# Kernel tuning notes

Hardware: AMD Instinct MI355X
Metric: run time of the kernel (lower is better)

The kernel has to match this reference:

```python
import jax, jax.numpy as jnp
import numpy as np

NF = 64   # num_feat
DG = 8    # deformable_groups (also conv groups)
B, H, W = 4, 96, 96
K = 9     # 3x3 kernel positions


def _conv(x, w, b, padding=1, dilation=1, groups=1):
    out = jax.lax.conv_general_dilated(
        x, w, (1, 1), [(padding, padding), (padding, padding)],
        rhs_dilation=(dilation, dilation),
        dimension_numbers=('NCHW', 'OIHW', 'NCHW'),
        feature_group_count=groups)
    return out + b[None, :, None, None]


def _lrelu(t):
    return jnp.where(t >= 0, t, 0.1 * t)


def _cat_align(a, b):
    # channel-interleaved concat: [a0,b0,a1,b1,...]
    Bn, k, h, w = a.shape
    return jnp.stack([a, b], axis=2).reshape(Bn, 2 * k, h, w)


def _deform_conv(x, offset, mask, weight, bias, dilation, padding):
    # DCNv2 modulated deformable conv, stride 1.
    Bn, C, h, w = x.shape
    Cpg = C // DG
    off = offset.reshape(Bn, DG, K, 2, h, w)          # (dy, dx) per group/kernel pos
    m = mask.reshape(Bn, DG, K, h, w)
    ky = (jnp.repeat(jnp.arange(3), 3) * dilation - padding).astype(x.dtype)  # (K,)
    kx = (jnp.tile(jnp.arange(3), 3) * dilation - padding).astype(x.dtype)
    hs = jnp.arange(h, dtype=x.dtype)
    ws = jnp.arange(w, dtype=x.dtype)
    py = off[:, :, :, 0] + ky[None, None, :, None, None] + hs[None, None, None, :, None]
    px = off[:, :, :, 1] + kx[None, None, :, None, None] + ws[None, None, None, None, :]
    y0f = jnp.floor(py); x0f = jnp.floor(px)
    ly = (py - y0f)[:, :, None]  # broadcast over Cpg
    lx = (px - x0f)[:, :, None]
    y0 = y0f.astype(jnp.int32); x0 = x0f.astype(jnp.int32)
    xg = x.reshape(Bn, DG, Cpg, h * w)

    def gather(yi, xi):
        inb = ((yi >= 0) & (yi < h) & (xi >= 0) & (xi < w))
        idx = (jnp.clip(yi, 0, h - 1) * w + jnp.clip(xi, 0, w - 1)).reshape(Bn, DG, 1, K * h * w)
        v = jnp.take_along_axis(xg, jnp.broadcast_to(idx, (Bn, DG, Cpg, K * h * w)), axis=3)
        return v.reshape(Bn, DG, Cpg, K, h, w) * inb[:, :, None].astype(x.dtype)

    v00 = gather(y0, x0); v01 = gather(y0, x0 + 1)
    v10 = gather(y0 + 1, x0); v11 = gather(y0 + 1, x0 + 1)
    val = (v00 * (1 - ly) * (1 - lx) + v01 * (1 - ly) * lx
           + v10 * ly * (1 - lx) + v11 * ly * lx) * m[:, :, None]
    sampled = val.reshape(Bn, C, K, h, w)
    out = jnp.einsum('bckhw,ock->bohw', sampled, weight.reshape(weight.shape[0], C, K))
    return out + bias[None, :, None, None]


def _dcn(x, off_feat, om_w, om_b, w, b, dilation):
    pad = dilation  # int(3/2)*dilation
    out = _conv(off_feat, om_w, om_b, padding=pad, dilation=dilation)
    o1, o2, msk = jnp.split(out, 3, axis=1)
    offset = jnp.concatenate([o1, o2], axis=1)
    mask = jax.nn.sigmoid(msk)
    return _deform_conv(x, offset, mask, w, b, dilation, pad)


def setup_inputs() -> dict:
    key = jax.random.key(0)
    ks = iter(jax.random.split(key, 64))
    def rn(shape, s=0.05):
        return jax.random.normal(next(ks), shape, jnp.float32) * s
    d = {}
    d['nbr_feat'] = jax.random.normal(next(ks), (B, NF, H, W), jnp.float32)
    d['ref_feat'] = jax.random.normal(next(ks), (B, NF, H, W), jnp.float32)
    for lv, has3 in [('l3', False), ('l2', True), ('l1', True)]:
        d[f'oc1_w_{lv}'] = rn((NF, 2 * NF // DG, 3, 3)); d[f'oc1_b_{lv}'] = rn((NF,))
        oc2_in = 2 * NF if has3 else NF
        d[f'oc2_w_{lv}'] = rn((NF, oc2_in // DG, 3, 3)); d[f'oc2_b_{lv}'] = rn((NF,))
        if has3:
            d[f'oc3_w_{lv}'] = rn((NF, NF // DG, 3, 3)); d[f'oc3_b_{lv}'] = rn((NF,))
            d[f'fc_w_{lv}'] = rn((NF, 2 * NF // DG, 3, 3)); d[f'fc_b_{lv}'] = rn((NF,))
        d[f'om_w_{lv}'] = rn((DG * 3 * K, NF, 3, 3), 0.01); d[f'om_b_{lv}'] = rn((DG * 3 * K,), 0.01)
        d[f'dcn_w_{lv}'] = rn((NF, NF, 3, 3)); d[f'dcn_b_{lv}'] = rn((NF,))
    d['cas_oc1_w'] = rn((NF, 2 * NF // DG, 3, 3)); d['cas_oc1_b'] = rn((NF,))
    d['cas_oc2_w'] = rn((NF, NF // DG, 3, 3)); d['cas_oc2_b'] = rn((NF,))
    d['cas_om_w'] = rn((DG * 3 * K, NF, 3, 3), 0.01); d['cas_om_b'] = rn((DG * 3 * K,), 0.01)
    d['cas_w'] = rn((NF, NF, 3, 3)); d['cas_b'] = rn((NF,))
    return d


def reference(nbr_feat, ref_feat,
              oc1_w_l3, oc1_b_l3, oc2_w_l3, oc2_b_l3, om_w_l3, om_b_l3, dcn_w_l3, dcn_b_l3,
              oc1_w_l2, oc1_b_l2, oc2_w_l2, oc2_b_l2, oc3_w_l2, oc3_b_l2, fc_w_l2, fc_b_l2,
              om_w_l2, om_b_l2, dcn_w_l2, dcn_b_l2,
              oc1_w_l1, oc1_b_l1, oc2_w_l1, oc2_b_l1, oc3_w_l1, oc3_b_l1, fc_w_l1, fc_b_l1,
              om_w_l1, om_b_l1, dcn_w_l1, dcn_b_l1,
              cas_oc1_w, cas_oc1_b, cas_oc2_w, cas_oc2_b, cas_om_w, cas_om_b, cas_w, cas_b):
    # level 3 (dilation 5)
    off = _lrelu(_conv(_cat_align(nbr_feat, ref_feat), oc1_w_l3, oc1_b_l3, groups=DG))
    off = _lrelu(_conv(off, oc2_w_l3, oc2_b_l3, groups=DG))
    feat = _lrelu(_dcn(nbr_feat, off, om_w_l3, om_b_l3, dcn_w_l3, dcn_b_l3, 5))
    to, tf = off, feat
    # level 2 (dilation 3)
    off = _lrelu(_conv(_cat_align(nbr_feat, ref_feat), oc1_w_l2, oc1_b_l2, groups=DG))
    off = _lrelu(_conv(_cat_align(off, to), oc2_w_l2, oc2_b_l2, groups=DG))
    off = _lrelu(_conv(off, oc3_w_l2, oc3_b_l2, groups=DG))
    feat = _dcn(nbr_feat, off, om_w_l2, om_b_l2, dcn_w_l2, dcn_b_l2, 3)
    feat = _lrelu(_conv(_cat_align(feat, tf), fc_w_l2, fc_b_l2, groups=DG))
    to, tf = off, feat
    # level 1 (dilation 1), no lrelu on feat
    off = _lrelu(_conv(_cat_align(nbr_feat, ref_feat), oc1_w_l1, oc1_b_l1, groups=DG))
    off = _lrelu(_conv(_cat_align(off, to), oc2_w_l1, oc2_b_l1, groups=DG))
    off = _lrelu(_conv(off, oc3_w_l1, oc3_b_l1, groups=DG))
    feat = _dcn(nbr_feat, off, om_w_l1, om_b_l1, dcn_w_l1, dcn_b_l1, 1)
    feat = _conv(_cat_align(feat, tf), fc_w_l1, fc_b_l1, groups=DG)
    # cascade
    off = _cat_align(feat, ref_feat)
    off = _lrelu(_conv(_lrelu(_conv(off, cas_oc1_w, cas_oc1_b, groups=DG)), cas_oc2_w, cas_oc2_b, groups=DG))
    feat = _lrelu(_dcn(feat, off, cas_om_w, cas_om_b, cas_w, cas_b, 1))
    return feat
```

## Files before the change

kernel.cpp:

```cpp
#include <hip/hip_runtime.h>

#define BATCH 4
#define NFEAT 64
#define DGRP 8
#define HH 96
#define WW 96
#define HWP (HH*WW)

typedef short short4a __attribute__((ext_vector_type(4)));
typedef short short8 __attribute__((ext_vector_type(8)));
typedef float f32x4 __attribute__((ext_vector_type(4)));
typedef float f32x16 __attribute__((ext_vector_type(16)));

__device__ inline short f2bf(float f) {
  union { float f; unsigned u; } v; v.f = f;
  unsigned r = v.u + 0x7fff + ((v.u >> 16) & 1);
  return (short)(r >> 16);
}
__device__ inline float bf2f(short s) {
  return __uint_as_float(((unsigned)(unsigned short)s) << 16);
}

__global__ __launch_bounds__(256) void prep_om(
    const float* __restrict__ s0, const float* __restrict__ s1,
    const float* __restrict__ s2, const float* __restrict__ s3,
    short* __restrict__ dst) {
  int gid = blockIdx.x * 256 + threadIdx.x;
  if (gid >= 4 * 147456) return;
  int t = gid / 147456, r = gid % 147456;
  int tile = r / 18432, r2 = r % 18432;
  int kk = r2 / 512, r3 = r2 % 512;
  int lane = r3 / 8, j = r3 % 8;
  int col = lane & 31, half = lane >> 5;
  int oc = tile * 32 + col;
  int k = kk * 16 + half * 8 + j;
  int p = k >> 6, c = k & 63;
  const float* s = (t == 0) ? s0 : (t == 1) ? s1 : (t == 2) ? s2 : s3;
  float v = (oc < 216) ? s[(size_t)oc * 576 + c * 9 + p] : 0.f;
  dst[gid] = f2bf(v);
}

__global__ __launch_bounds__(256) void prep_dcnw(
    const float* __restrict__ s0, const float* __restrict__ s1,
    const float* __restrict__ s2, const float* __restrict__ s3,
    short* __restrict__ dst) {
  int gid = blockIdx.x * 256 + threadIdx.x;
  if (gid >= 4 * 36864) return;
  int t = gid / 36864, r = gid % 36864;
  int tile = r / 18432, r2 = r % 18432;
  int kk = r2 / 512, r3 = r2 % 512;
  int lane = r3 / 8, j = r3 % 8;
  int col = lane & 31, half = lane >> 5;
  int oc = tile * 32 + col;
  int k = kk * 16 + half * 8 + j;
  int p = k >> 6, c = k & 63;
  const float* s = (t == 0) ? s0 : (t == 1) ? s1 : (t == 2) ? s2 : s3;
  dst[gid] = f2bf(s[(size_t)oc * 576 + c * 9 + p]);
}

struct GwArgs {
  const float* src[12];
  int cat[12];
  int base[13];
};

__global__ __launch_bounds__(256) void prep_gw(GwArgs a, short* __restrict__ dst) {
  int gid = blockIdx.x * 256 + threadIdx.x;
  if (gid >= a.base[12]) return;
  int t = 0;
  while (gid >= a.base[t + 1]) ++t;
  int r = gid - a.base[t];
  const float* s = a.src[t];
  const int tsz = a.cat[t] ? 4608 : 2560;
  int tile = r / tsz, r2 = r % tsz;
  int kk = r2 / 512, r3 = r2 % 512;
  int lane = r3 >> 3, j = r3 & 7;
  int m = lane & 15, quad = lane >> 4;
  int oc = tile * 16 + m;
  int j32 = quad * 8 + j;
  float val = 0.f;
  if (a.cat[t]) {
    int gsel = j32 >> 4, ssel = (j32 >> 3) & 1, ch8 = j32 & 7;
    if (gsel == (m >> 3)) val = s[oc * 144 + (2 * ch8 + ssel) * 9 + kk];
  } else {
    int tapsel = j32 >> 4, gsel = (j32 >> 3) & 1, ch8 = j32 & 7;
    int p = 2 * kk + tapsel;
    if (p < 9 && gsel == (m >> 3)) val = s[oc * 72 + ch8 * 9 + p];
  }
  dst[gid] = f2bf(val);
}

__global__ __launch_bounds__(256) void transpose_bf16(
    const float* __restrict__ in0, short* __restrict__ out0,
    const float* __restrict__ in1, short* __restrict__ out1) {
  const float* in = blockIdx.z ? in1 : in0;
  short* out = blockIdx.z ? out1 : out0;
  __shared__ float s[64][65];
  const int p0 = blockIdx.x * 64;
  const int b = blockIdx.y;
  const int tx = threadIdx.x, ty = threadIdx.y;
  for (int c = ty; c < 64; c += 4)
    s[c][tx] = in[((size_t)b * NFEAT + c) * HWP + p0 + tx];
  __syncthreads();
  for (int p = ty; p < 64; p += 4)
    out[((size_t)b * HWP + p0 + p) * NFEAT + tx] = f2bf(s[tx][p]);
}

template <bool CAT, bool LRELU>
__global__ __launch_bounds__(256) void gconv_mfma(
    const short* __restrict__ in0, const short* __restrict__ in1,
    const short* __restrict__ Wsh, const float* __restrict__ bias,
    short* __restrict__ out) {
  const int lane = threadIdx.x, t = threadIdx.y;
  const int n = lane & 15, quad = lane >> 4;
  const int pixbase = blockIdx.x * 32;
  const int b = blockIdx.y;
  constexpr int NKK = CAT ? 9 : 5;

  short8 A[NKK];
#pragma unroll
  for (int kk = 0; kk < NKK; ++kk)
    A[kk] = *(const short8*)(Wsh + ((size_t)(t * NKK + kk) * 64 + lane) * 8);

  const short* sb;
  if (CAT) {
    sb = ((quad & 1) ? in1 : in0) + (size_t)b * HWP * 64 + (2 * t + (quad >> 1)) * 8;
  } else {
    sb = in0 + (size_t)b * HWP * 64 + (2 * t + (quad & 1)) * 8;
  }

  f32x4 acc[2] = {};
#pragma unroll
  for (int nt = 0; nt < 2; ++nt) {
    const int pix = pixbase + nt * 16 + n;
    const int yp = pix / WW, xp = pix % WW;
#pragma unroll
    for (int kk = 0; kk < NKK; ++kk) {
      const int p = CAT ? kk : (2 * kk + (quad >> 1));
      short8 B = {0, 0, 0, 0, 0, 0, 0, 0};
      if (p < 9) {
        const int sy = yp + p / 3 - 1, sx = xp + p % 3 - 1;
        if (((unsigned)sy < (unsigned)HH) && ((unsigned)sx < (unsigned)WW))
          B = *(const short8*)(sb + (size_t)(sy * WW + sx) * 64);
      }
      acc[nt] = __builtin_amdgcn_mfma_f32_16x16x32_bf16(A[kk], B, acc[nt], 0, 0, 0);
    }
  }

  const int ocb = t * 16 + quad * 4;
  const float b0 = bias[ocb], b1 = bias[ocb + 1], b2 = bias[ocb + 2], b3 = bias[ocb + 3];
#pragma unroll
  for (int nt = 0; nt < 2; ++nt) {
    float v0 = acc[nt][0] + b0, v1 = acc[nt][1] + b1;
    float v2 = acc[nt][2] + b2, v3 = acc[nt][3] + b3;
    if (LRELU) {
      v0 = (v0 >= 0.f) ? v0 : 0.1f * v0;
      v1 = (v1 >= 0.f) ? v1 : 0.1f * v1;
      v2 = (v2 >= 0.f) ? v2 : 0.1f * v2;
      v3 = (v3 >= 0.f) ? v3 : 0.1f * v3;
    }
    short4a pk = {f2bf(v0), f2bf(v1), f2bf(v2), f2bf(v3)};
    *(short4a*)(out + ((size_t)b * HWP + pixbase + nt * 16 + n) * 64 + ocb) = pk;
  }
}

#define BPITCH 324
template <int D>
__global__ __launch_bounds__(256) void omconv_mfma(
    const short* __restrict__ pixT,
    const short* __restrict__ Wsh,
    const float* __restrict__ bias,
    short* __restrict__ out) {
  const int lane = threadIdx.x;
  const int w = threadIdx.y;
  const int lid = w * 64 + lane;
  const int col = lane & 31, half = lane >> 5;
  const int pixbase = blockIdx.x * 64;
  const int b = blockIdx.y;

  __shared__ short Bs[64 * BPITCH];

  const short* aP0 = Wsh + ((size_t)(w * 36) * 64) * 8 + (size_t)lane * 8;
  const short* aP1 = Wsh + ((size_t)((w + 4) * 36) * 64) * 8 + (size_t)lane * 8;
  const short* pixb = pixT + (size_t)b * HWP * 64;

  f32x16 acc00 = {}, acc01 = {}, acc10 = {}, acc11 = {};

  for (int ph = 0; ph < 2; ++ph) {
    const int ntap = ph ? 4 : 5, pbase = ph ? 5 : 0, kbase = ph ? 20 : 0;
    if (ph) __syncthreads();
    const int nchunk = 64 * ntap * 8;
    for (int i = lid; i < nchunk; i += 256) {
      int row = i / (ntap * 8), q = i % (ntap * 8);
      int p = pbase + (q >> 3), c8 = q & 7;
      int pix = pixbase + row;
      int yp = pix / WW, xp = pix % WW;
      int sy = yp + (p / 3 - 1) * D, sx = xp + (p % 3 - 1) * D;
      short4a lo = {0, 0, 0, 0}, hi = {0, 0, 0, 0};
      if (((unsigned)sy < (unsigned)HH) && ((unsigned)sx < (unsigned)WW)) {
        const short* src = pixb + (size_t)(sy * WW + sx) * 64 + c8 * 8;
        lo = *(const short4a*)src;
        hi = *(const short4a*)(src + 4);
      }
      short* dst = Bs + row * BPITCH + q * 8;
      *(short4a*)dst = lo;
      *(short4a*)(dst + 4) = hi;
    }
    __syncthreads();

    const int nkk = ntap * 4;
#pragma unroll 4
    for (int kk = 0; kk < nkk; ++kk) {
      const int kkg = kbase + kk;
      short8 A0 = *(const short8*)(aP0 + (size_t)kkg * 512);
      short8 A1 = *(const short8*)(aP1 + (size_t)kkg * 512);
      const short* b0 = Bs + col * BPITCH + kk * 16 + half * 8;
      const short* b1 = Bs + (32 + col) * BPITCH + kk * 16 + half * 8;
      short4a l0 = *(const short4a*)b0, h0 = *(const short4a*)(b0 + 4);
      short4a l1 = *(const short4a*)b1, h1 = *(const short4a*)(b1 + 4);
      short8 B0 = {l0[0], l0[1], l0[2], l0[3], h0[0], h0[1], h0[2], h0[3]};
      short8 B1 = {l1[0], l1[1], l1[2], l1[3], h1[0], h1[1], h1[2], h1[3]};
      acc00 = __builtin_amdgcn_mfma_f32_32x32x16_bf16(A0, B0, acc00, 0, 0, 0);
      acc01 = __builtin_amdgcn_mfma_f32_32x32x16_bf16(A0, B1, acc01, 0, 0, 0);
      acc10 = __builtin_amdgcn_mfma_f32_32x32x16_bf16(A1, B0, acc10, 0, 0, 0);
      acc11 = __builtin_amdgcn_mfma_f32_32x32x16_bf16(A1, B1, acc11, 0, 0, 0);
    }
  }

  const int pix0 = pixbase + col, pix1 = pixbase + 32 + col;
#pragma unroll
  for (int r = 0; r < 16; ++r) {
    const int rrow = (r & 3) + 8 * (r >> 2) + 4 * half;
    const int oc0 = w * 32 + rrow;
    const int oc1 = (w + 4) * 32 + rrow;
    const float bs0 = bias[oc0];
    out[((size_t)b * 216 + oc0) * HWP + pix0] = f2bf(acc00[r] + bs0);
    out[((size_t)b * 216 + oc0) * HWP + pix1] = f2bf(acc01[r] + bs0);
    if (oc1 < 216) {
      const float bs1 = bias[oc1];
      out[((size_t)b * 216 + oc1) * HWP + pix0] = f2bf(acc10[r] + bs1);
      out[((size_t)b * 216 + oc1) * HWP + pix1] = f2bf(acc11[r] + bs1);
    }
  }
}

template <int D, bool LRELU, bool PMOUT>
__global__ __launch_bounds__(256) void dcn_fused(
    const short* __restrict__ xT,
    const short* __restrict__ om,
    const short* __restrict__ Wd,
    const float* __restrict__ bias,
    void* __restrict__ outv) {
  __shared__ short Ls[36 * 512];
  __shared__ float red[2][64][17];
  const int tx = threadIdx.x, ty = threadIdx.y;
  const int pb = blockIdx.x, b = blockIdx.y;

  {
    const int px = tx, dg = ty;
    const int pix = pb * 32 + px;
    const int yp = pix / WW, xp = pix % WW;
    const size_t bOM = (size_t)b * 216 * HWP;
    const short* xb = xT + (size_t)b * HWP * 64 + dg * 8;
    short* Sp = Ls + (size_t)((dg & 1) * 32 + px) * 8;

#pragma unroll
    for (int k = 0; k < 9; ++k) {
      float dy = bf2f(om[bOM + (size_t)(dg * 18 + 2 * k) * HWP + pix]);
      float dxv = bf2f(om[bOM + (size_t)(dg * 18 + 2 * k + 1) * HWP + pix]);
      float mr = bf2f(om[bOM + (size_t)(144 + dg * 9 + k) * HWP + pix]);
      float m = 1.f / (1.f + __expf(-mr));
      float py = (float)(yp + (k / 3 - 1) * D) + dy;
      float px_ = (float)(xp + (k % 3 - 1) * D) + dxv;
      float y0f = floorf(py), x0f = floorf(px_);
      float ly = py - y0f, lx = px_ - x0f;
      int y0 = (int)y0f, x0 = (int)x0f;
      int y1 = y0 + 1, x1 = x0 + 1;
      bool vy0 = (unsigned)y0 < (unsigned)HH, vy1 = (unsigned)y1 < (unsigned)HH;
      bool vx0 = (unsigned)x0 < (unsigned)WW, vx1 = (unsigned)x1 < (unsigned)WW;
      int cy0 = min(max(y0, 0), HH - 1), cy1 = min(max(y1, 0), HH - 1);
      int cx0 = min(max(x0, 0), WW - 1), cx1 = min(max(x1, 0), WW - 1);
      float w00 = (vy0 && vx0) ? (1.f - ly) * (1.f - lx) * m : 0.f;
      float w01 = (vy0 && vx1) ? (1.f - ly) * lx * m : 0.f;
      float w10 = (vy1 && vx0) ? ly * (1.f - lx) * m : 0.f;
      float w11 = (vy1 && vx1) ? ly * lx * m : 0.f;
      short8 s00 = *(const short8*)(xb + (size_t)(cy0 * WW + cx0) * 64);
      short8 s01 = *(const short8*)(xb + (size_t)(cy0 * WW + cx1) * 64);
      short8 s10 = *(const short8*)(xb + (size_t)(cy1 * WW + cx0) * 64);
      short8 s11 = *(const short8*)(xb + (size_t)(cy1 * WW + cx1) * 64);
      short8 pk;
#pragma unroll
      for (int cl = 0; cl < 8; ++cl) {
        float v = w00 * bf2f(s00[cl]) + w01 * bf2f(s01[cl]) +
                  w10 * bf2f(s10[cl]) + w11 * bf2f(s11[cl]);
        pk[cl] = f2bf(v);
      }
      const int kk = k * 4 + (dg >> 1);
      *(short8*)(Sp + (size_t)kk * 512) = pk;
    }
  }
  __syncthreads();

  const int lid = ty * 32 + tx;
  const int lane = lid & 63, w = lid >> 6;
  const int col = lane & 31, half = lane >> 5;
  const int octile = w & 1, kh = w >> 1;
  const int pix = pb * 32 + col;

  const short* aP = Wd + ((size_t)(octile * 36) * 64 + lane) * 8;
  const short* bP = Ls + (size_t)lane * 8;

  f32x16 acc = {};
#pragma unroll 6
  for (int kk = 0; kk < 18; ++kk) {
    const int kkg = kh * 18 + kk;
    short8 A = *(const short8*)(aP + (size_t)kkg * 512);
    short8 B = *(const short8*)(bP + (size_t)kkg * 512);
    acc = __builtin_amdgcn_mfma_f32_32x32x16_bf16(A, B, acc, 0, 0, 0);
  }

  if (kh == 1) {
#pragma unroll
    for (int r = 0; r < 16; ++r) red[octile][lane][r] = acc[r];
  }
  __syncthreads();
  if (kh == 0) {
    if (PMOUT) {
      short* out = (short*)outv;
#pragma unroll
      for (int rg = 0; rg < 4; ++rg) {
        short4a pk;
#pragma unroll
        for (int i = 0; i < 4; ++i) {
          const int r = rg * 4 + i;
          const int oc = octile * 32 + i + 8 * rg + 4 * half;
          float v = acc[r] + red[octile][lane][r] + bias[oc];
          if (LRELU) v = (v >= 0.f) ? v : 0.1f * v;
          pk[i] = f2bf(v);
        }
        *(short4a*)(out + ((size_t)b * HWP + pix) * 64 + octile * 32 + 8 * rg + 4 * half) = pk;
      }
    } else {
      float* out = (float*)outv;
#pragma unroll
      for (int r = 0; r < 16; ++r) {
        const int oc = octile * 32 + (r & 3) + 8 * (r >> 2) + 4 * half;
        float v = acc[r] + red[octile][lane][r] + bias[oc];
        if (LRELU) v = (v >= 0.f) ? v : 0.1f * v;
        out[((size_t)b * NFEAT + oc) * HWP + pix] = v;
      }
    }
  }
}

extern "C" void kernel_launch(void* const* d_in, const int* in_sizes, int n_in,
                              void* d_out, int out_size, void* d_ws, size_t ws_size,
                              hipStream_t stream) {
  const float* nbr = (const float*)d_in[0];
  const float* ref = (const float*)d_in[1];
  auto f = [&](int i) { return (const float*)d_in[i]; };

  short* s0 = (short*)d_ws;
  const size_t PM = (size_t)BATCH * HWP * 64;
  short* omB = s0;
  short* refT = omB + 7962624;
  short* pmA = refT + PM;
  short* pmB = pmA + PM;
  short* pmC = pmB + PM;
  short* pmD = pmC + PM;
  short* pmE = pmD + PM;
  short* wbf = pmE + PM;
  short* wdcn = wbf + 589824;
  short* wgc = wdcn + 147456;
  short* nbrT = (short*)d_out;

  prep_om<<<(4 * 147456 + 255) / 256, 256, 0, stream>>>(f(6), f(18), f(30), f(38), wbf);
  prep_dcnw<<<(4 * 36864 + 255) / 256, 256, 0, stream>>>(f(8), f(20), f(32), f(40), wdcn);

  static const int gSrc[12] = {2, 4, 10, 12, 14, 16, 22, 24, 26, 28, 34, 36};
  static const int gCat[12] = {1, 0, 1, 1, 0, 1, 1, 1, 0, 1, 1, 0};
  GwArgs ga;
  int gb = 0;
  const short* wg[12];
  for (int t = 0; t < 12; ++t) {
    ga.src[t] = f(gSrc[t]);
    ga.cat[t] = gCat[t];
    ga.base[t] = gb;
    wg[t] = wgc + gb;
    gb += gCat[t] ? 18432 : 10240;
  }
  ga.base[12] = gb;
  prep_gw<<<(gb + 255) / 256, 256, 0, stream>>>(ga, wgc);

  short* wbf_l3 = wbf;
  short* wbf_l2 = wbf + 147456;
  short* wbf_l1 = wbf + 2 * 147456;
  short* wbf_cas = wbf + 3 * 147456;
  short* wd_l3 = wdcn;
  short* wd_l2 = wdcn + 36864;
  short* wd_l1 = wdcn + 2 * 36864;
  short* wd_cas = wdcn + 3 * 36864;

  dim3 gcGrid(288, BATCH), gcBlk(64, 4);
  dim3 omGrid(144, BATCH), omBlk(64, 4);
  dim3 dfGrid(288, BATCH), dfBlk(32, 8);
  dim3 trGrid(HWP / 64, BATCH, 2), trBlk(64, 4);

  transpose_bf16<<<trGrid, trBlk, 0, stream>>>(nbr, nbrT, ref, refT);

  gconv_mfma<true, true><<<gcGrid, gcBlk, 0, stream>>>(nbrT, refT, wg[0], f(3), pmA);
  gconv_mfma<false, true><<<gcGrid, gcBlk, 0, stream>>>(pmA, nullptr, wg[1], f(5), pmB);
  omconv_mfma<5><<<omGrid, omBlk, 0, stream>>>(pmB, wbf_l3, f(7), omB);
  dcn_fused<5, true, true><<<dfGrid, dfBlk, 0, stream>>>(nbrT, omB, wd_l3, f(9), pmC);

  gconv_mfma<true, true><<<gcGrid, gcBlk, 0, stream>>>(nbrT, refT, wg[2], f(11), pmA);
  gconv_mfma<true, true><<<gcGrid, gcBlk, 0, stream>>>(pmA, pmB, wg[3], f(13), pmD);
  gconv_mfma<false, true><<<gcGrid, gcBlk, 0, stream>>>(pmD, nullptr, wg[4], f(15), pmE);
  omconv_mfma<3><<<omGrid, omBlk, 0, stream>>>(pmE, wbf_l2, f(19), omB);
  dcn_fused<3, false, true><<<dfGrid, dfBlk, 0, stream>>>(nbrT, omB, wd_l2, f(21), pmD);
  gconv_mfma<true, true><<<gcGrid, gcBlk, 0, stream>>>(pmD, pmC, wg[5], f(17), pmA);

  gconv_mfma<true, true><<<gcGrid, gcBlk, 0, stream>>>(nbrT, refT, wg[6], f(23), pmC);
  gconv_mfma<true, true><<<gcGrid, gcBlk, 0, stream>>>(pmC, pmE, wg[7], f(25), pmD);
  gconv_mfma<false, true><<<gcGrid, gcBlk, 0, stream>>>(pmD, nullptr, wg[8], f(27), pmC);
  omconv_mfma<1><<<omGrid, omBlk, 0, stream>>>(pmC, wbf_l1, f(31), omB);
  dcn_fused<1, false, true><<<dfGrid, dfBlk, 0, stream>>>(nbrT, omB, wd_l1, f(33), pmD);
  gconv_mfma<true, false><<<gcGrid, gcBlk, 0, stream>>>(pmD, pmA, wg[9], f(29), pmB);

  gconv_mfma<true, true><<<gcGrid, gcBlk, 0, stream>>>(pmB, refT, wg[10], f(35), pmC);
  gconv_mfma<false, true><<<gcGrid, gcBlk, 0, stream>>>(pmC, nullptr, wg[11], f(37), pmD);
  omconv_mfma<1><<<omGrid, omBlk, 0, stream>>>(pmD, wbf_cas, f(39), omB);
  dcn_fused<1, true, false><<<dfGrid, dfBlk, 0, stream>>>(pmB, omB, wd_cas, f(41), (float*)d_out);
}
```

Baseline: 528.1 us.

## Stage grouped-conv taps in LDS, batch the three oc1 convs, shrink omconv tiles

Grouped 3x3 convs now cooperatively load a 16-pixel im2col tile into shared memory before the MFMA loop, instead of each lane doing scattered global loads per tap. The three level oc1 convs, which all read nbr/ref, are launched as one kernel over a z-dimension, using two extra workspace buffers. The buffer assignments for levels 2 and 1 are reshuffled to match. The offset/mask conv switches from 64-pixel tiles loaded in two phases to 32-pixel tiles loaded in one pass. The smaller tiles double the grid size and raise parallelism, at the cost of less weight reuse per block and more launch blocks.

```diff
diff --git a/kernel.cpp b/kernel.cpp
--- a/kernel.cpp
+++ b/kernel.cpp
@@ -107,140 +107,163 @@
 }
 
 template <bool CAT, bool LRELU>
+__device__ __forceinline__ void gconv_body(
+    const short* __restrict__ in0, const short* __restrict__ in1,
+    const short* __restrict__ Wsh, const float* __restrict__ bias,
+    short* __restrict__ out, int pixbase, int b) {
+  constexpr int NKK = CAT ? 9 : 5;
+  constexpr int NC8 = CAT ? 16 : 8;
+  constexpr int NTAP = CAT ? 9 : 10;
+  constexpr int PITCH = CAT ? 1156 : 644;
+  __shared__ short Ls[16 * PITCH];
+
+  const int lane = threadIdx.x, t = threadIdx.y;
+  const int n = lane & 15, quad = lane >> 4;
+  const int lid = t * 64 + lane;
+
+  const size_t bofs = (size_t)b * HWP * 64;
+  for (int i = lid; i < 16 * NTAP * NC8; i += 256) {
+    int row = i / (NTAP * NC8), q = i % (NTAP * NC8);
+    int p = q / NC8, vc8 = q % NC8;
+    short4a lo = {0, 0, 0, 0}, hi = {0, 0, 0, 0};
+    if (p < 9) {
+      int pix = pixbase + row;
+      int yp = pix / WW, xp = pix % WW;
+      int sy = yp + p / 3 - 1, sx = xp + p % 3 - 1;
+      if (((unsigned)sy < (unsigned)HH) && ((unsigned)sx < (unsigned)WW)) {
+        const short* src;
+        int c8;
+        if (CAT) {
+          src = (vc8 & 1) ? in1 : in0;
+          c8 = vc8 >> 1;
+        } else {
+          src = in0;
+          c8 = vc8;
+        }
+        const short* sp = src + bofs + (size_t)(sy * WW + sx) * 64 + c8 * 8;
+        lo = *(const short4a*)sp;
+        hi = *(const short4a*)(sp + 4);
+      }
+    }
+    short* dst = Ls + row * PITCH + q * 8;
+    *(short4a*)dst = lo;
+    *(short4a*)(dst + 4) = hi;
+  }
+  __syncthreads();
+
+  short8 A[NKK];
+#pragma unroll
+  for (int kk = 0; kk < NKK; ++kk)
+    A[kk] = *(const short8*)(Wsh + ((size_t)(t * NKK + kk) * 64 + lane) * 8);
+
+  f32x4 acc = {};
+#pragma unroll
+  for (int kk = 0; kk < NKK; ++kk) {
+    int colo;
+    if (CAT) {
+      colo = kk * 128 + (4 * t + quad) * 8;
+    } else {
+      int p = 2 * kk + (quad >> 1);
+      colo = p * 64 + (2 * t + (quad & 1)) * 8;
+    }
+    const short* bp = Ls + n * PITCH + colo;
+    short4a l = *(const short4a*)bp, h = *(const short4a*)(bp + 4);
+    short8 B = {l[0], l[1], l[2], l[3], h[0], h[1], h[2], h[3]};
+    acc = __builtin_amdgcn_mfma_f32_16x16x32_bf16(A[kk], B, acc, 0, 0, 0);
+  }
+
+  const int ocb = t * 16 + quad * 4;
+  float v0 = acc[0] + bias[ocb], v1 = acc[1] + bias[ocb + 1];
+  float v2 = acc[2] + bias[ocb + 2], v3 = acc[3] + bias[ocb + 3];
+  if (LRELU) {
+    v0 = (v0 >= 0.f) ? v0 : 0.1f * v0;
+    v1 = (v1 >= 0.f) ? v1 : 0.1f * v1;
+    v2 = (v2 >= 0.f) ? v2 : 0.1f * v2;
+    v3 = (v3 >= 0.f) ? v3 : 0.1f * v3;
+  }
+  short4a pk = {f2bf(v0), f2bf(v1), f2bf(v2), f2bf(v3)};
+  *(short4a*)(out + ((size_t)b * HWP + pixbase + n) * 64 + ocb) = pk;
+}
+
+template <bool CAT, bool LRELU>
 __global__ __launch_bounds__(256) void gconv_mfma(
     const short* __restrict__ in0, const short* __restrict__ in1,
     const short* __restrict__ Wsh, const float* __restrict__ bias,
     short* __restrict__ out) {
-  const int lane = threadIdx.x, t = threadIdx.y;
-  const int n = lane & 15, quad = lane >> 4;
-  const int pixbase = blockIdx.x * 32;
-  const int b = blockIdx.y;
-  constexpr int NKK = CAT ? 9 : 5;
-
-  short8 A[NKK];
-#pragma unroll
-  for (int kk = 0; kk < NKK; ++kk)
-    A[kk] = *(const short8*)(Wsh + ((size_t)(t * NKK + kk) * 64 + lane) * 8);
-
-  const short* sb;
-  if (CAT) {
-    sb = ((quad & 1) ? in1 : in0) + (size_t)b * HWP * 64 + (2 * t + (quad >> 1)) * 8;
-  } else {
-    sb = in0 + (size_t)b * HWP * 64 + (2 * t + (quad & 1)) * 8;
-  }
-
-  f32x4 acc[2] = {};
-#pragma unroll
-  for (int nt = 0; nt < 2; ++nt) {
-    const int pix = pixbase + nt * 16 + n;
-    const int yp = pix / WW, xp = pix % WW;
-#pragma unroll
-    for (int kk = 0; kk < NKK; ++kk) {
-      const int p = CAT ? kk : (2 * kk + (quad >> 1));
-      short8 B = {0, 0, 0, 0, 0, 0, 0, 0};
-      if (p < 9) {
-        const int sy = yp + p / 3 - 1, sx = xp + p % 3 - 1;
-        if (((unsigned)sy < (unsigned)HH) && ((unsigned)sx < (unsigned)WW))
-          B = *(const short8*)(sb + (size_t)(sy * WW + sx) * 64);
-      }
-      acc[nt] = __builtin_amdgcn_mfma_f32_16x16x32_bf16(A[kk], B, acc[nt], 0, 0, 0);
-    }
-  }
-
-  const int ocb = t * 16 + quad * 4;
-  const float b0 = bias[ocb], b1 = bias[ocb + 1], b2 = bias[ocb + 2], b3 = bias[ocb + 3];
-#pragma unroll
-  for (int nt = 0; nt < 2; ++nt) {
-    float v0 = acc[nt][0] + b0, v1 = acc[nt][1] + b1;
-    float v2 = acc[nt][2] + b2, v3 = acc[nt][3] + b3;
-    if (LRELU) {
-      v0 = (v0 >= 0.f) ? v0 : 0.1f * v0;
-      v1 = (v1 >= 0.f) ? v1 : 0.1f * v1;
-      v2 = (v2 >= 0.f) ? v2 : 0.1f * v2;
-      v3 = (v3 >= 0.f) ? v3 : 0.1f * v3;
-    }
-    short4a pk = {f2bf(v0), f2bf(v1), f2bf(v2), f2bf(v3)};
-    *(short4a*)(out + ((size_t)b * HWP + pixbase + nt * 16 + n) * 64 + ocb) = pk;
-  }
-}
-
-#define BPITCH 324
+  gconv_body<CAT, LRELU>(in0, in1, Wsh, bias, out, blockIdx.x * 16, blockIdx.y);
+}
+
+struct Oc1Args {
+  const short* W[3];
+  const float* bias[3];
+  short* out[3];
+};
+
+__global__ __launch_bounds__(256) void gconv_oc1x3(
+    const short* __restrict__ in0, const short* __restrict__ in1, Oc1Args a) {
+  const int job = blockIdx.z;
+  gconv_body<true, true>(in0, in1, a.W[job], a.bias[job], a.out[job],
+                         blockIdx.x * 16, blockIdx.y);
+}
+
+#define OPITCH 580
 template <int D>
 __global__ __launch_bounds__(256) void omconv_mfma(
     const short* __restrict__ pixT,
     const short* __restrict__ Wsh,
     const float* __restrict__ bias,
     short* __restrict__ out) {
-  const int lane = threadIdx.x;
-  const int w = threadIdx.y;
+  const int lane = threadIdx.x, w = threadIdx.y;
   const int lid = w * 64 + lane;
   const int col = lane & 31, half = lane >> 5;
-  const int pixbase = blockIdx.x * 64;
+  const int pixbase = blockIdx.x * 32;
   const int b = blockIdx.y;
 
-  __shared__ short Bs[64 * BPITCH];
-
-  const short* aP0 = Wsh + ((size_t)(w * 36) * 64) * 8 + (size_t)lane * 8;
-  const short* aP1 = Wsh + ((size_t)((w + 4) * 36) * 64) * 8 + (size_t)lane * 8;
+  __shared__ short Bs[32 * OPITCH];
+
   const short* pixb = pixT + (size_t)b * HWP * 64;
-
-  f32x16 acc00 = {}, acc01 = {}, acc10 = {}, acc11 = {};
-
-  for (int ph = 0; ph < 2; ++ph) {
-    const int ntap = ph ? 4 : 5, pbase = ph ? 5 : 0, kbase = ph ? 20 : 0;
-    if (ph) __syncthreads();
-    const int nchunk = 64 * ntap * 8;
-    for (int i = lid; i < nchunk; i += 256) {
-      int row = i / (ntap * 8), q = i % (ntap * 8);
-      int p = pbase + (q >> 3), c8 = q & 7;
-      int pix = pixbase + row;
-      int yp = pix / WW, xp = pix % WW;
-      int sy = yp + (p / 3 - 1) * D, sx = xp + (p % 3 - 1) * D;
-      short4a lo = {0, 0, 0, 0}, hi = {0, 0, 0, 0};
-      if (((unsigned)sy < (unsigned)HH) && ((unsigned)sx < (unsigned)WW)) {
-        const short* src = pixb + (size_t)(sy * WW + sx) * 64 + c8 * 8;
-        lo = *(const short4a*)src;
-        hi = *(const short4a*)(src + 4);
-      }
-      short* dst = Bs + row * BPITCH + q * 8;
-      *(short4a*)dst = lo;
-      *(short4a*)(dst + 4) = hi;
+  for (int i = lid; i < 32 * 72; i += 256) {
+    int row = i / 72, q = i % 72;
+    int p = q >> 3, c8 = q & 7;
+    int pix = pixbase + row;
+    int yp = pix / WW, xp = pix % WW;
+    int sy = yp + (p / 3 - 1) * D, sx = xp + (p % 3 - 1) * D;
+    short4a lo = {0, 0, 0, 0}, hi = {0, 0, 0, 0};
+    if (((unsigned)sy < (unsigned)HH) && ((unsigned)sx < (unsigned)WW)) {
+      const short* src = pixb + (size_t)(sy * WW + sx) * 64 + c8 * 8;
+      lo = *(const short4a*)src;
+      hi = *(const short4a*)(src + 4);
     }
-    __syncthreads();
-
-    const int nkk = ntap * 4;
-#pragma unroll 4
-    for (int kk = 0; kk < nkk; ++kk) {
-      const int kkg = kbase + kk;
-      short8 A0 = *(const short8*)(aP0 + (size_t)kkg * 512);
-      short8 A1 = *(const short8*)(aP1 + (size_t)kkg * 512);
-      const short* b0 = Bs + col * BPITCH + kk * 16 + half * 8;
-      const short* b1 = Bs + (32 + col) * BPITCH + kk * 16 + half * 8;
-      short4a l0 = *(const short4a*)b0, h0 = *(const short4a*)(b0 + 4);
-      short4a l1 = *(const short4a*)b1, h1 = *(const short4a*)(b1 + 4);
-      short8 B0 = {l0[0], l0[1], l0[2], l0[3], h0[0], h0[1], h0[2], h0[3]};
-      short8 B1 = {l1[0], l1[1], l1[2], l1[3], h1[0], h1[1], h1[2], h1[3]};
-      acc00 = __builtin_amdgcn_mfma_f32_32x32x16_bf16(A0, B0, acc00, 0, 0, 0);
-      acc01 = __builtin_amdgcn_mfma_f32_32x32x16_bf16(A0, B1, acc01, 0, 0, 0);
-      acc10 = __builtin_amdgcn_mfma_f32_32x32x16_bf16(A1, B0, acc10, 0, 0, 0);
-      acc11 = __builtin_amdgcn_mfma_f32_32x32x16_bf16(A1, B1, acc11, 0, 0, 0);
-    }
-  }
-
-  const int pix0 = pixbase + col, pix1 = pixbase + 32 + col;
+    short* dst = Bs + row * OPITCH + q * 8;
+    *(short4a*)dst = lo;
+    *(short4a*)(dst + 4) = hi;
+  }
+  __syncthreads();
+
+  const short* aP0 = Wsh + ((size_t)(w * 36) * 64 + lane) * 8;
+  const short* aP1 = Wsh + ((size_t)((w + 4) * 36) * 64 + lane) * 8;
+
+  f32x16 acc0 = {}, acc1 = {};
+#pragma unroll 6
+  for (int kk = 0; kk < 36; ++kk) {
+    short8 A0 = *(const short8*)(aP0 + (size_t)kk * 512);
+    short8 A1 = *(const short8*)(aP1 + (size_t)kk * 512);
+    const short* bp = Bs + col * OPITCH + kk * 16 + half * 8;
+    short4a l = *(const short4a*)bp, h = *(const short4a*)(bp + 4);
+    short8 B = {l[0], l[1], l[2], l[3], h[0], h[1], h[2], h[3]};
+    acc0 = __builtin_amdgcn_mfma_f32_32x32x16_bf16(A0, B, acc0, 0, 0, 0);
+    acc1 = __builtin_amdgcn_mfma_f32_32x32x16_bf16(A1, B, acc1, 0, 0, 0);
+  }
+
+  const int pix = pixbase + col;
 #pragma unroll
   for (int r = 0; r < 16; ++r) {
     const int rrow = (r & 3) + 8 * (r >> 2) + 4 * half;
     const int oc0 = w * 32 + rrow;
     const int oc1 = (w + 4) * 32 + rrow;
-    const float bs0 = bias[oc0];
-    out[((size_t)b * 216 + oc0) * HWP + pix0] = f2bf(acc00[r] + bs0);
-    out[((size_t)b * 216 + oc0) * HWP + pix1] = f2bf(acc01[r] + bs0);
-    if (oc1 < 216) {
-      const float bs1 = bias[oc1];
-      out[((size_t)b * 216 + oc1) * HWP + pix0] = f2bf(acc10[r] + bs1);
-      out[((size_t)b * 216 + oc1) * HWP + pix1] = f2bf(acc11[r] + bs1);
-    }
+    out[((size_t)b * 216 + oc0) * HWP + pix] = f2bf(acc0[r] + bias[oc0]);
+    if (oc1 < 216)
+      out[((size_t)b * 216 + oc1) * HWP + pix] = f2bf(acc1[r] + bias[oc1]);
   }
 }
 
@@ -369,7 +392,9 @@
   short* pmC = pmB + PM;
   short* pmD = pmC + PM;
   short* pmE = pmD + PM;
-  short* wbf = pmE + PM;
+  short* pmF = pmE + PM;
+  short* pmG = pmF + PM;
+  short* wbf = pmG + PM;
   short* wdcn = wbf + 589824;
   short* wgc = wdcn + 147456;
   short* nbrT = (short*)d_out;
@@ -401,28 +426,32 @@
   short* wd_l1 = wdcn + 2 * 36864;
   short* wd_cas = wdcn + 3 * 36864;
 
-  dim3 gcGrid(288, BATCH), gcBlk(64, 4);
-  dim3 omGrid(144, BATCH), omBlk(64, 4);
+  dim3 gcGrid(576, BATCH), gcBlk(64, 4);
+  dim3 oc1Grid(576, BATCH, 3);
+  dim3 omGrid(288, BATCH), omBlk(64, 4);
   dim3 dfGrid(288, BATCH), dfBlk(32, 8);
   dim3 trGrid(HWP / 64, BATCH, 2), trBlk(64, 4);
 
   transpose_bf16<<<trGrid, trBlk, 0, stream>>>(nbr, nbrT, ref, refT);
 
-  gconv_mfma<true, true><<<gcGrid, gcBlk, 0, stream>>>(nbrT, refT, wg[0], f(3), pmA);
+  Oc1Args oa;
+  oa.W[0] = wg[0]; oa.bias[0] = f(3);  oa.out[0] = pmA;
+  oa.W[1] = wg[2]; oa.bias[1] = f(11); oa.out[1] = pmF;
+  oa.W[2] = wg[6]; oa.bias[2] = f(23); oa.out[2] = pmG;
+  gconv_oc1x3<<<oc1Grid, gcBlk, 0, stream>>>(nbrT, refT, oa);
+
   gconv_mfma<false, true><<<gcGrid, gcBlk, 0, stream>>>(pmA, nullptr, wg[1], f(5), pmB);
   omconv_mfma<5><<<omGrid, omBlk, 0, stream>>>(pmB, wbf_l3, f(7), omB);
   dcn_fused<5, true, true><<<dfGrid, dfBlk, 0, stream>>>(nbrT, omB, wd_l3, f(9), pmC);
 
-  gconv_mfma<true, true><<<gcGrid, gcBlk, 0, stream>>>(nbrT, refT, wg[2], f(11), pmA);
-  gconv_mfma<true, true><<<gcGrid, gcBlk, 0, stream>>>(pmA, pmB, wg[3], f(13), pmD);
+  gconv_mfma<true, true><<<gcGrid, gcBlk, 0, stream>>>(pmF, pmB, wg[3], f(13), pmD);
   gconv_mfma<false, true><<<gcGrid, gcBlk, 0, stream>>>(pmD, nullptr, wg[4], f(15), pmE);
   omconv_mfma<3><<<omGrid, omBlk, 0, stream>>>(pmE, wbf_l2, f(19), omB);
   dcn_fused<3, false, true><<<dfGrid, dfBlk, 0, stream>>>(nbrT, omB, wd_l2, f(21), pmD);
   gconv_mfma<true, true><<<gcGrid, gcBlk, 0, stream>>>(pmD, pmC, wg[5], f(17), pmA);
 
-  gconv_mfma<true, true><<<gcGrid, gcBlk, 0, stream>>>(nbrT, refT, wg[6], f(23), pmC);
-  gconv_mfma<true, true><<<gcGrid, gcBlk, 0, stream>>>(pmC, pmE, wg[7], f(25), pmD);
-  gconv_mfma<false, true><<<gcGrid, gcBlk, 0, stream>>>(pmD, nullptr, wg[8], f(27), pmC);
+  gconv_mfma<true, true><<<gcGrid, gcBlk, 0, stream>>>(pmG, pmE, wg[7], f(25), pmB);
+  gconv_mfma<false, true><<<gcGrid, gcBlk, 0, stream>>>(pmB, nullptr, wg[8], f(27), pmC);
   omconv_mfma<1><<<omGrid, omBlk, 0, stream>>>(pmC, wbf_l1, f(31), omB);
   dcn_fused<1, false, true><<<dfGrid, dfBlk, 0, stream>>>(nbrT, omB, wd_l1, f(33), pmD);
   gconv_mfma<true, false><<<gcGrid, gcBlk, 0, stream>>>(pmD, pmA, wg[9], f(29), pmB);
```

New measurement: 567.2 us. 1.07x slower.
